# Performance work log

Hardware: AMD Instinct MI355X
Metric: run time of the kernel (lower is better)

Reference implementation:

```python
import jax, jax.numpy as jnp
import numpy as np

# Solver constants (from HopfieldLayer.__init__ / RKF56Solver(dt, tol=0.01, min_dt=0.1))
DT0 = 0.1
TOL = 0.01
MIN_DT = 0.1
MAX_STEPS = 32       # cap on adaptive iterations (fixed-length scan, masked)
SPEED_TOL = 1e-3     # stop_condition: |dx/dt|_inf below this => converged


def inverse_boundary_reflect(x):
    # y = x on even integer cells, 1 - x on odd cells; plain autodiff gives the
    # same VJP as the tf.custom_gradient (dy vs -dy) since the int cast is
    # only used in the predicate.
    i = x.astype(jnp.int32)
    return jnp.where(i % 2 == 0, x, 1.0 - x)


def make_pvf(W, b):
    def energy(y):
        # classic Hopfield energy, summed over batch: -0.5 y^T W y - b.y
        return -0.5 * jnp.einsum('bi,ij,bj->', y, W, y) - jnp.sum(y @ b)

    def pvf(x):  # phase vector field: -grad_x E(G^{-1}(x))
        return -jax.grad(lambda z: energy(inverse_boundary_reflect(z)))(x)

    return pvf


def _hopfield_forward(x0, W, b):
    f = make_pvf(W, b)

    def body(carry, _):
        x, dt, t, done = carry
        # Runge-Kutta-Fehlberg 6-stage embedded pair (4th/5th order)
        k1 = f(x)
        k2 = f(x + dt * (0.25 * k1))
        k3 = f(x + dt * (3.0 / 32.0 * k1 + 9.0 / 32.0 * k2))
        k4 = f(x + dt * (1932.0 / 2197.0 * k1 - 7200.0 / 2197.0 * k2 + 7296.0 / 2197.0 * k3))
        k5 = f(x + dt * (439.0 / 216.0 * k1 - 8.0 * k2 + 3680.0 / 513.0 * k3 - 845.0 / 4104.0 * k4))
        k6 = f(x + dt * (-8.0 / 27.0 * k1 + 2.0 * k2 - 3544.0 / 2565.0 * k3 + 1859.0 / 4104.0 * k4 - 11.0 / 40.0 * k5))
        x5 = x + dt * (16.0 / 135.0 * k1 + 6656.0 / 12825.0 * k3 + 28561.0 / 56430.0 * k4 - 9.0 / 50.0 * k5 + 2.0 / 55.0 * k6)
        x4 = x + dt * (25.0 / 216.0 * k1 + 1408.0 / 2565.0 * k3 + 2197.0 / 4104.0 * k4 - 1.0 / 5.0 * k5)
        err = jnp.max(jnp.abs(x5 - x4))
        accept = err < TOL
        step = jnp.logical_and(accept, jnp.logical_not(done))
        x_new = jnp.where(step, x5, x)
        t_new = jnp.where(step, t + dt, t)
        # stop condition: effective speed of accepted step below threshold
        speed = jnp.max(jnp.abs(x5 - x)) / dt
        done_new = jnp.logical_or(done, jnp.logical_and(step, speed < SPEED_TOL))
        # adaptive step-size control (non-differentiable, as in the TF solver)
        scale = 0.9 * (TOL / (jax.lax.stop_gradient(err) + 1e-12)) ** 0.2
        dt_new = jnp.maximum(dt * jnp.clip(scale, 0.1, 4.0), MIN_DT)
        dt_new = jnp.where(done, dt, dt_new)
        return (x_new, dt_new, t_new, done_new), None

    init = (x0,
            jnp.asarray(DT0, x0.dtype),
            jnp.asarray(0.0, x0.dtype),
            jnp.asarray(False))
    (x1, _, _, _), _ = jax.lax.scan(body, init, None, length=MAX_STEPS)
    return x1


def setup_inputs() -> dict:
    key = jax.random.key(0)
    kx, kw, kb = jax.random.split(key, 3)
    B, D = 512, 2048
    x0 = jax.random.uniform(kx, (B, D), dtype=jnp.float32)
    W = jax.random.normal(kw, (D, D), dtype=jnp.float32) / np.sqrt(D)
    W = 0.5 * (W + W.T)  # symmetric Hopfield coupling
    b = 0.1 * jax.random.normal(kb, (D,), dtype=jnp.float32)
    return {"x0": x0, "W": W, "b": b}


def reference(x0, W, b):
    return _hopfield_forward(x0, W, b)
```

## Files before the change

kernel.cpp:

```cpp
#include <hip/hip_runtime.h>

#define DDIM 2048
#define BDIM 512
#define NELEM (BDIM * DDIM)
#define NV4 (NELEM / 4)
#define NW4 (DDIM * DDIM / 4)

#define SC_DT 0
#define SC_DONE 1
#define SC_ERR 2
#define SC_SP 3
#define SC_COMMIT 4

#define TOLF 0.01f
#define MIN_DTF 0.1f
#define SPEED_TOLF 1e-3f

typedef _Float16 half8 __attribute__((ext_vector_type(8)));
typedef _Float16 half4v __attribute__((ext_vector_type(4)));
typedef float f32x4 __attribute__((ext_vector_type(4)));

__device__ __forceinline__ void glds16(const _Float16* g, _Float16* l) {
    __builtin_amdgcn_global_load_lds((__attribute__((address_space(1))) void*)g,
                                     (__attribute__((address_space(3))) void*)l, 16, 0, 0);
}

__device__ __forceinline__ void split_f16(float y, _Float16& h, _Float16& l) {
    h = (_Float16)y;
    l = (_Float16)(y - (float)h);
}

__device__ __forceinline__ float reflect_f(float v) {
    int i = (int)v;
    return ((i & 1) == 0) ? v : 1.0f - v;
}


__global__ void wconv_kernel(const float* __restrict__ W, _Float16* __restrict__ Wh,
                             _Float16* __restrict__ Wl) {
    int tid = blockIdx.x * blockDim.x + threadIdx.x;
    const float4* Wv = (const float4*)W;
    for (int i = tid; i < NW4; i += gridDim.x * blockDim.x) {
        float4 v = Wv[i];
        half4v h, l;
        float vv[4] = {v.x, v.y, v.z, v.w};
#pragma unroll
        for (int q = 0; q < 4; ++q) {
            _Float16 hh, ll;
            split_f16(vv[q], hh, ll);
            h[q] = hh;
            l[q] = ll;
        }
        *(half4v*)&Wh[(size_t)i * 4] = h;
        *(half4v*)&Wl[(size_t)i * 4] = l;
    }
}

__global__ void init_kernel(const float* __restrict__ x0, float* __restrict__ x,
                            _Float16* __restrict__ Ah, _Float16* __restrict__ Al,
                            float* __restrict__ scal) {
    int tid = blockIdx.x * blockDim.x + threadIdx.x;
    const float4* X0 = (const float4*)x0;
    float4* X = (float4*)x;
    for (int i = tid; i < NV4; i += gridDim.x * blockDim.x) {
        float4 v = X0[i];
        X[i] = v;
        half4v h, l;
        float vv[4] = {v.x, v.y, v.z, v.w};
#pragma unroll
        for (int q = 0; q < 4; ++q) {
            float y = reflect_f(vv[q]);
            _Float16 hh, ll;
            split_f16(y, hh, ll);
            h[q] = hh;
            l[q] = ll;
        }
        *(half4v*)&Ah[(size_t)i * 4] = h;
        *(half4v*)&Al[(size_t)i * 4] = l;
    }
    if (tid == 0) {
        scal[SC_DT] = 0.1f;
        ((unsigned int*)scal)[SC_DONE] = 0u;
        scal[SC_ERR] = 0.0f;
        scal[SC_SP] = 0.0f;
        ((unsigned int*)scal)[SC_COMMIT] = 0u;
    }
}


template <int S>
__global__ __launch_bounds__(512, 2) void stage_kernel(
    const _Float16* __restrict__ Ah, const _Float16* __restrict__ Al,
    _Float16* __restrict__ Aoh, _Float16* __restrict__ Aol, const _Float16* __restrict__ Wh,
    const _Float16* __restrict__ Wl, const float* __restrict__ bias,
    const float* __restrict__ xg, const float* __restrict__ gk1, const float* __restrict__ gk2,
    const float* __restrict__ gk3, const float* __restrict__ gk4, const float* __restrict__ gk5,
    float* __restrict__ kout, float* __restrict__ x5out, float* __restrict__ scal) {
    __shared__ __align__(16) _Float16 lds[2][2][4][64 * 64];
    __shared__ float serr[8], ssp[8];

    const int tid = threadIdx.x;
    const int li = tid & 63;
    const int wid = tid >> 6;
    const int g = wid >> 2;
    const int w4 = wid & 3;
    const int wm = w4 >> 1, wn = w4 & 1;

    const int bid = blockIdx.x;
    const int xcd = bid & 7, jj = bid >> 3;
    const int bm = (xcd & 1) * 4 + (jj & 3);
    const int bn = (xcd >> 1) * 8 + (jj >> 2);

    f32x4 acc[2][2];
#pragma unroll
    for (int a = 0; a < 2; ++a)
#pragma unroll
        for (int b = 0; b < 2; ++b) acc[a][b] = (f32x4)(0.0f);

    auto stage4 = [&](int buf, int k0) {
#pragma unroll
        for (int cc = 0; cc < 2; ++cc) {
            int c = w4 + cc * 4;
            int row = c * 8 + (li >> 3);
            int clog = (li & 7) ^ (row & 7);
            int ga = (bm * 64 + row) * DDIM + k0 + clog * 8;
            int gw = (bn * 64 + row) * DDIM + k0 + clog * 8;
            int lo = c * 512 + li * 8;
            glds16(Ah + ga, &lds[g][buf][0][lo]);
            glds16(Al + ga, &lds[g][buf][1][lo]);
            glds16(Wh + gw, &lds[g][buf][2][lo]);
            glds16(Wl + gw, &lds[g][buf][3][lo]);
        }
    };

    auto rdfrag = [&](int buf, int mat, int rbase, int ks) -> half8 {
        int r = rbase + (li & 15);
        int cl = ks * 4 + (li >> 4);
        int off = r * 64 + ((cl ^ (r & 7)) << 3);
        return *(const half8*)&lds[g][buf][mat][off];
    };

    auto compute = [&](int buf) {
#pragma unroll
        for (int ks = 0; ks < 2; ++ks) {
            half8 ah[2], al[2], bh[2], bl[2];
#pragma unroll
            for (int f = 0; f < 2; ++f) {
                ah[f] = rdfrag(buf, 0, wm * 32 + f * 16, ks);
                al[f] = rdfrag(buf, 1, wm * 32 + f * 16, ks);
                bh[f] = rdfrag(buf, 2, wn * 32 + f * 16, ks);
                bl[f] = rdfrag(buf, 3, wn * 32 + f * 16, ks);
            }
#pragma unroll
            for (int mi = 0; mi < 2; ++mi)
#pragma unroll
                for (int ni = 0; ni < 2; ++ni) {
                    acc[mi][ni] = __builtin_amdgcn_mfma_f32_16x16x32_f16(ah[mi], bh[ni],
                                                                         acc[mi][ni], 0, 0, 0);
                    acc[mi][ni] = __builtin_amdgcn_mfma_f32_16x16x32_f16(ah[mi], bl[ni],
                                                                         acc[mi][ni], 0, 0, 0);
                    acc[mi][ni] = __builtin_amdgcn_mfma_f32_16x16x32_f16(al[mi], bh[ni],
                                                                         acc[mi][ni], 0, 0, 0);
                }
        }
    };

    const int kbase = g * 1024;
    stage4(0, kbase);
#pragma unroll 2
    for (int t = 0; t < 16; ++t) {
        if (t + 1 < 16) {
            stage4((t + 1) & 1, kbase + (t + 1) * 64);
            asm volatile("s_waitcnt vmcnt(8)" ::: "memory");
        } else {
            asm volatile("s_waitcnt vmcnt(0)" ::: "memory");
        }
        __builtin_amdgcn_sched_barrier(0);
        __builtin_amdgcn_s_barrier();
        compute(t & 1);
        __builtin_amdgcn_s_barrier();
    }

    float4* xch = (float4*)&lds[0][0][0][0];
#pragma unroll
    for (int ni = 0; ni < 2; ++ni) {
        int slot = ((g * 4 + w4) * 2 + ni) * 64 + li;
        if (g == 0)
            xch[slot] = make_float4(acc[1][ni][0], acc[1][ni][1], acc[1][ni][2], acc[1][ni][3]);
        else
            xch[slot] = make_float4(acc[0][ni][0], acc[0][ni][1], acc[0][ni][2], acc[0][ni][3]);
    }
    __syncthreads();
    f32x4 fin[2];
#pragma unroll
    for (int ni = 0; ni < 2; ++ni) {
        int slot = (((1 - g) * 4 + w4) * 2 + ni) * 64 + li;
        float4 p = xch[slot];
        f32x4 mine = (g == 0) ? acc[0][ni] : acc[1][ni];
        mine[0] += p.x;
        mine[1] += p.y;
        mine[2] += p.z;
        mine[3] += p.w;
        fin[ni] = mine;
    }

    const float dt = scal[SC_DT];
    const int lrow = li >> 4, lcol = li & 15;
    const float bias0 = bias[bn * 64 + wn * 32 + lcol];
    const float bias1 = bias[bn * 64 + wn * 32 + 16 + lcol];
    float lerr = 0.0f, lsp = 0.0f;

#pragma unroll
    for (int r = 0; r < 4; ++r) {
        int m = bm * 64 + wm * 32 + g * 16 + lrow * 4 + r;
        size_t base = (size_t)m * DDIM;
#pragma unroll
        for (int ni = 0; ni < 2; ++ni) {
            int n = bn * 64 + wn * 32 + ni * 16 + lcol;
            size_t idx = base + n;
            float accv = fin[ni][r] + (ni == 0 ? bias0 : bias1);
            float xv = xg[idx];
            float lk1 = 0.f, lk2 = 0.f, lk3 = 0.f, lk4 = 0.f, lk5 = 0.f;
            if constexpr (S >= 2) lk1 = gk1[idx];
            if constexpr (S >= 3) lk2 = gk2[idx];
            if constexpr (S >= 4) lk3 = gk3[idx];
            if constexpr (S >= 5) lk4 = gk4[idx];
            if constexpr (S >= 6) lk5 = gk5[idx];
            float xs;
            if constexpr (S == 1) xs = xv;
            if constexpr (S == 2) xs = xv + dt * (0.25f * lk1);
            if constexpr (S == 3)
                xs = xv + dt * ((float)(3.0 / 32.0) * lk1 + (float)(9.0 / 32.0) * lk2);
            if constexpr (S == 4)
                xs = xv + dt * ((float)(1932.0 / 2197.0) * lk1 + (float)(-7200.0 / 2197.0) * lk2 +
                                (float)(7296.0 / 2197.0) * lk3);
            if constexpr (S == 5)
                xs = xv + dt * ((float)(439.0 / 216.0) * lk1 - 8.0f * lk2 +
                                (float)(3680.0 / 513.0) * lk3 + (float)(-845.0 / 4104.0) * lk4);
            if constexpr (S == 6)
                xs = xv + dt * ((float)(-8.0 / 27.0) * lk1 + 2.0f * lk2 +
                                (float)(-3544.0 / 2565.0) * lk3 + (float)(1859.0 / 4104.0) * lk4 +
                                (float)(-11.0 / 40.0) * lk5);
            float sgn = (((int)xs) & 1) ? -1.0f : 1.0f;
            float kv = sgn * accv;
            if constexpr (S < 6) {
                kout[idx] = kv;
                float xn;
                if constexpr (S == 1) xn = xv + dt * (0.25f * kv);
                if constexpr (S == 2)
                    xn = xv + dt * ((float)(3.0 / 32.0) * lk1 + (float)(9.0 / 32.0) * kv);
                if constexpr (S == 3)
                    xn = xv + dt * ((float)(1932.0 / 2197.0) * lk1 +
                                    (float)(-7200.0 / 2197.0) * lk2 + (float)(7296.0 / 2197.0) * kv);
                if constexpr (S == 4)
                    xn = xv + dt * ((float)(439.0 / 216.0) * lk1 - 8.0f * lk2 +
                                    (float)(3680.0 / 513.0) * lk3 + (float)(-845.0 / 4104.0) * kv);
                if constexpr (S == 5)
                    xn = xv + dt * ((float)(-8.0 / 27.0) * lk1 + 2.0f * lk2 +
                                    (float)(-3544.0 / 2565.0) * lk3 +
                                    (float)(1859.0 / 4104.0) * lk4 + (float)(-11.0 / 40.0) * kv);
                float y = reflect_f(xn);
                _Float16 hh, ll;
                split_f16(y, hh, ll);
                Aoh[idx] = hh;
                Aol[idx] = ll;
            } else {
                float x5 = xv + dt * ((float)(16.0 / 135.0) * lk1 + (float)(6656.0 / 12825.0) * lk3 +
                                      (float)(28561.0 / 56430.0) * lk4 + (float)(-9.0 / 50.0) * lk5 +
                                      (float)(2.0 / 55.0) * kv);
                float x4 = xv + dt * ((float)(25.0 / 216.0) * lk1 + (float)(1408.0 / 2565.0) * lk3 +
                                      (float)(2197.0 / 4104.0) * lk4 + (float)(-1.0 / 5.0) * lk5);
                lerr = fmaxf(lerr, fabsf(x5 - x4));
                lsp = fmaxf(lsp, fabsf(x5 - xv));
                x5out[idx] = x5;
            }
        }
    }

    if constexpr (S == 6) {
#pragma unroll
        for (int off = 32; off > 0; off >>= 1) {
            lerr = fmaxf(lerr, __shfl_down(lerr, off));
            lsp = fmaxf(lsp, __shfl_down(lsp, off));
        }
        if (li == 0) {
            serr[wid] = lerr;
            ssp[wid] = lsp;
        }
        __syncthreads();
        if (tid == 0) {
            float e = serr[0], s = ssp[0];
#pragma unroll
            for (int w = 1; w < 8; ++w) {
                e = fmaxf(e, serr[w]);
                s = fmaxf(s, ssp[w]);
            }
            atomicMax((unsigned int*)&scal[SC_ERR], __float_as_uint(e));
            atomicMax((unsigned int*)&scal[SC_SP], __float_as_uint(s));
        }
    }
}


__global__ void scalar_update(float* scal) {
    if (threadIdx.x == 0 && blockIdx.x == 0) {
        float dt = scal[SC_DT];
        float err = scal[SC_ERR];
        float spmax = scal[SC_SP];
        unsigned int done = ((unsigned int*)scal)[SC_DONE];
        bool accept = err < TOLF;
        bool step = accept && (done == 0u);
        float speed = spmax / dt;
        unsigned int done_new = (done || (step && (speed < SPEED_TOLF))) ? 1u : 0u;
        float scale = 0.9f * powf(TOLF / (err + 1e-12f), 0.2f);
        scale = fminf(fmaxf(scale, 0.1f), 4.0f);
        float dtn = fmaxf(dt * scale, MIN_DTF);
        scal[SC_DT] = done ? dt : dtn;
        ((unsigned int*)scal)[SC_DONE] = done_new;
        ((unsigned int*)scal)[SC_COMMIT] = step ? 1u : 0u;
        scal[SC_ERR] = 0.0f;
        scal[SC_SP] = 0.0f;
    }
}

__global__ void commit_prep(float* __restrict__ x, const float* __restrict__ x5,
                            _Float16* __restrict__ Ah, _Float16* __restrict__ Al,
                            const float* __restrict__ scal) {
    bool com = ((const unsigned int*)scal)[SC_COMMIT] != 0u;
    int tid = blockIdx.x * blockDim.x + threadIdx.x;
    float4* X = (float4*)x;
    const float4* X5 = (const float4*)x5;
    for (int i = tid; i < NV4; i += gridDim.x * blockDim.x) {
        float4 v = com ? X5[i] : X[i];
        if (com) X[i] = v;
        half4v h, l;
        float vv[4] = {v.x, v.y, v.z, v.w};
#pragma unroll
        for (int q = 0; q < 4; ++q) {
            float y = reflect_f(vv[q]);
            _Float16 hh, ll;
            split_f16(y, hh, ll);
            h[q] = hh;
            l[q] = ll;
        }
        *(half4v*)&Ah[(size_t)i * 4] = h;
        *(half4v*)&Al[(size_t)i * 4] = l;
    }
}


extern "C" void kernel_launch(void* const* d_in, const int* in_sizes, int n_in, void* d_out,
                              int out_size, void* d_ws, size_t ws_size, hipStream_t stream) {
    const float* x0 = (const float*)d_in[0];
    const float* W = (const float*)d_in[1];
    const float* bias = (const float*)d_in[2];
    float* x = (float*)d_out;

    float* ws = (float*)d_ws;
    float* k1 = ws + 0 * (size_t)NELEM;
    float* k2 = ws + 1 * (size_t)NELEM;
    float* k3 = ws + 2 * (size_t)NELEM;
    float* k4 = ws + 3 * (size_t)NELEM;
    float* k5 = ws + 4 * (size_t)NELEM;
    float* x5 = ws + 5 * (size_t)NELEM;
    float* scal = ws + 6 * (size_t)NELEM;
    _Float16* hb = (_Float16*)(ws + 6 * (size_t)NELEM + 64);
    _Float16* A0h = hb + 0 * (size_t)NELEM;
    _Float16* A0l = hb + 1 * (size_t)NELEM;
    _Float16* A1h = hb + 2 * (size_t)NELEM;
    _Float16* A1l = hb + 3 * (size_t)NELEM;
    _Float16* Wh = hb + 4 * (size_t)NELEM;
    _Float16* Wl = Wh + (size_t)DDIM * DDIM;

    wconv_kernel<<<2048, 256, 0, stream>>>(W, Wh, Wl);
    init_kernel<<<1024, 256, 0, stream>>>(x0, x, A1h, A1l, scal);

    for (int it = 0; it < 32; ++it) {
        stage_kernel<1><<<256, 512, 0, stream>>>(A1h, A1l, A0h, A0l, Wh, Wl, bias, x, k1, k2, k3,
                                                 k4, k5, k1, x5, scal);
        stage_kernel<2><<<256, 512, 0, stream>>>(A0h, A0l, A1h, A1l, Wh, Wl, bias, x, k1, k2, k3,
                                                 k4, k5, k2, x5, scal);
        stage_kernel<3><<<256, 512, 0, stream>>>(A1h, A1l, A0h, A0l, Wh, Wl, bias, x, k1, k2, k3,
                                                 k4, k5, k3, x5, scal);
        stage_kernel<4><<<256, 512, 0, stream>>>(A0h, A0l, A1h, A1l, Wh, Wl, bias, x, k1, k2, k3,
                                                 k4, k5, k4, x5, scal);
        stage_kernel<5><<<256, 512, 0, stream>>>(A1h, A1l, A0h, A0l, Wh, Wl, bias, x, k1, k2, k3,
                                                 k4, k5, k5, x5, scal);
        stage_kernel<6><<<256, 512, 0, stream>>>(A0h, A0l, A1h, A1l, Wh, Wl, bias, x, k1, k2, k3,
                                                 k4, k5, k1, x5, scal);
        scalar_update<<<1, 64, 0, stream>>>(scal);
        commit_prep<<<1024, 256, 0, stream>>>(x, x5, A1h, A1l, scal);
    }
}
```

Baseline: 4.139 ms.

## Load low-half fragments directly to registers, fuse scalar update into commit

The low-precision halves of A and W no longer go through LDS. Each wave loads them straight from global memory into registers as MFMA fragments, and only the high halves are staged via global_load_lds. This halves LDS footprint and LDS read traffic, and adds s_setprio around the MFMA blocks. The scalar_update kernel is folded into the commit kernel using ping-pong scalar slots, and commit is skipped entirely on rejected steps because the x-derived fp16 buffer is kept separate from the stage ping-pong buffers. The direct global loads are less coalesced and add register pressure.

```diff
diff --git a/kernel.cpp b/kernel.cpp
--- a/kernel.cpp
+++ b/kernel.cpp
@@ -10,7 +10,6 @@
 #define SC_DONE 1
 #define SC_ERR 2
 #define SC_SP 3
-#define SC_COMMIT 4
 
 #define TOLF 0.01f
 #define MIN_DTF 0.1f
@@ -57,7 +56,7 @@
 }
 
 __global__ void init_kernel(const float* __restrict__ x0, float* __restrict__ x,
-                            _Float16* __restrict__ Ah, _Float16* __restrict__ Al,
+                            _Float16* __restrict__ Axh, _Float16* __restrict__ Axl,
                             float* __restrict__ scal) {
     int tid = blockIdx.x * blockDim.x + threadIdx.x;
     const float4* X0 = (const float4*)x0;
@@ -75,15 +74,16 @@
             h[q] = hh;
             l[q] = ll;
         }
-        *(half4v*)&Ah[(size_t)i * 4] = h;
-        *(half4v*)&Al[(size_t)i * 4] = l;
+        *(half4v*)&Axh[(size_t)i * 4] = h;
+        *(half4v*)&Axl[(size_t)i * 4] = l;
     }
     if (tid == 0) {
         scal[SC_DT] = 0.1f;
         ((unsigned int*)scal)[SC_DONE] = 0u;
         scal[SC_ERR] = 0.0f;
         scal[SC_SP] = 0.0f;
-        ((unsigned int*)scal)[SC_COMMIT] = 0u;
+        scal[8 + SC_ERR] = 0.0f;
+        scal[8 + SC_SP] = 0.0f;
     }
 }
 
@@ -96,7 +96,7 @@
     const float* __restrict__ xg, const float* __restrict__ gk1, const float* __restrict__ gk2,
     const float* __restrict__ gk3, const float* __restrict__ gk4, const float* __restrict__ gk5,
     float* __restrict__ kout, float* __restrict__ x5out, float* __restrict__ scal) {
-    __shared__ __align__(16) _Float16 lds[2][2][4][64 * 64];
+    __shared__ __align__(16) _Float16 lds[2][2][2][64 * 64];
     __shared__ float serr[8], ssp[8];
 
     const int tid = threadIdx.x;
@@ -111,13 +111,20 @@
     const int bm = (xcd & 1) * 4 + (jj & 3);
     const int bn = (xcd >> 1) * 8 + (jj >> 2);
 
+    const int kbase = g * 1024;
+
     f32x4 acc[2][2];
 #pragma unroll
     for (int a = 0; a < 2; ++a)
 #pragma unroll
         for (int b = 0; b < 2; ++b) acc[a][b] = (f32x4)(0.0f);
 
-    auto stage4 = [&](int buf, int k0) {
+    const _Float16* Al_base =
+        Al + (size_t)(bm * 64 + wm * 32 + (li & 15)) * DDIM + kbase + ((li >> 4) << 3);
+    const _Float16* Wl_base =
+        Wl + (size_t)(bn * 64 + wn * 32 + (li & 15)) * DDIM + kbase + ((li >> 4) << 3);
+
+    auto stage_hi = [&](int buf, int k0) {
 #pragma unroll
         for (int cc = 0; cc < 2; ++cc) {
             int c = w4 + cc * 4;
@@ -125,11 +132,21 @@
             int clog = (li & 7) ^ (row & 7);
             int ga = (bm * 64 + row) * DDIM + k0 + clog * 8;
             int gw = (bn * 64 + row) * DDIM + k0 + clog * 8;
-            int lo = c * 512 + li * 8;
-            glds16(Ah + ga, &lds[g][buf][0][lo]);
-            glds16(Al + ga, &lds[g][buf][1][lo]);
-            glds16(Wh + gw, &lds[g][buf][2][lo]);
-            glds16(Wl + gw, &lds[g][buf][3][lo]);
+            int lo_ = c * 512 + li * 8;
+            glds16(Ah + ga, &lds[g][buf][0][lo_]);
+            glds16(Wh + gw, &lds[g][buf][1][lo_]);
+        }
+    };
+
+    auto load_lo = [&](half8(&lo)[8], int t) {
+#pragma unroll
+        for (int ks = 0; ks < 2; ++ks) {
+#pragma unroll
+            for (int mi = 0; mi < 2; ++mi)
+                lo[ks * 2 + mi] = *(const half8*)(Al_base + (size_t)mi * 16 * DDIM + t * 64 + ks * 32);
+#pragma unroll
+            for (int ni = 0; ni < 2; ++ni)
+                lo[4 + ks * 2 + ni] = *(const half8*)(Wl_base + (size_t)ni * 16 * DDIM + t * 64 + ks * 32);
         }
     };
 
@@ -140,44 +157,54 @@
         return *(const half8*)&lds[g][buf][mat][off];
     };
 
-    auto compute = [&](int buf) {
+    auto compute = [&](int buf, half8(&lo)[8]) {
 #pragma unroll
         for (int ks = 0; ks < 2; ++ks) {
-            half8 ah[2], al[2], bh[2], bl[2];
+            half8 ah[2], bh[2];
 #pragma unroll
             for (int f = 0; f < 2; ++f) {
                 ah[f] = rdfrag(buf, 0, wm * 32 + f * 16, ks);
-                al[f] = rdfrag(buf, 1, wm * 32 + f * 16, ks);
-                bh[f] = rdfrag(buf, 2, wn * 32 + f * 16, ks);
-                bl[f] = rdfrag(buf, 3, wn * 32 + f * 16, ks);
+                bh[f] = rdfrag(buf, 1, wn * 32 + f * 16, ks);
             }
+            __builtin_amdgcn_s_setprio(1);
 #pragma unroll
             for (int mi = 0; mi < 2; ++mi)
 #pragma unroll
                 for (int ni = 0; ni < 2; ++ni) {
                     acc[mi][ni] = __builtin_amdgcn_mfma_f32_16x16x32_f16(ah[mi], bh[ni],
                                                                          acc[mi][ni], 0, 0, 0);
-                    acc[mi][ni] = __builtin_amdgcn_mfma_f32_16x16x32_f16(ah[mi], bl[ni],
-                                                                         acc[mi][ni], 0, 0, 0);
-                    acc[mi][ni] = __builtin_amdgcn_mfma_f32_16x16x32_f16(al[mi], bh[ni],
-                                                                         acc[mi][ni], 0, 0, 0);
+                    acc[mi][ni] = __builtin_amdgcn_mfma_f32_16x16x32_f16(
+                        ah[mi], lo[4 + ks * 2 + ni], acc[mi][ni], 0, 0, 0);
+                    acc[mi][ni] = __builtin_amdgcn_mfma_f32_16x16x32_f16(
+                        lo[ks * 2 + mi], bh[ni], acc[mi][ni], 0, 0, 0);
                 }
+            __builtin_amdgcn_s_setprio(0);
         }
     };
 
-    const int kbase = g * 1024;
-    stage4(0, kbase);
-#pragma unroll 2
-    for (int t = 0; t < 16; ++t) {
-        if (t + 1 < 16) {
-            stage4((t + 1) & 1, kbase + (t + 1) * 64);
-            asm volatile("s_waitcnt vmcnt(8)" ::: "memory");
+    half8 loA[8], loB[8];
+    stage_hi(0, kbase);
+    load_lo(loA, 0);
+#pragma unroll 1
+    for (int tt = 0; tt < 8; ++tt) {
+        const int t0 = tt * 2;
+        stage_hi(1, kbase + (t0 + 1) * 64);
+        load_lo(loB, t0 + 1);
+        asm volatile("s_waitcnt vmcnt(12)" ::: "memory");
+        __builtin_amdgcn_sched_barrier(0);
+        __builtin_amdgcn_s_barrier();
+        compute(0, loA);
+        __builtin_amdgcn_s_barrier();
+        if (tt < 7) {
+            stage_hi(0, kbase + (t0 + 2) * 64);
+            load_lo(loA, t0 + 2);
+            asm volatile("s_waitcnt vmcnt(12)" ::: "memory");
         } else {
             asm volatile("s_waitcnt vmcnt(0)" ::: "memory");
         }
         __builtin_amdgcn_sched_barrier(0);
         __builtin_amdgcn_s_barrier();
-        compute(t & 1);
+        compute(1, loB);
         __builtin_amdgcn_s_barrier();
     }
 
@@ -302,37 +329,33 @@
 }
 
 
-__global__ void scalar_update(float* scal) {
-    if (threadIdx.x == 0 && blockIdx.x == 0) {
-        float dt = scal[SC_DT];
-        float err = scal[SC_ERR];
-        float spmax = scal[SC_SP];
-        unsigned int done = ((unsigned int*)scal)[SC_DONE];
-        bool accept = err < TOLF;
-        bool step = accept && (done == 0u);
-        float speed = spmax / dt;
-        unsigned int done_new = (done || (step && (speed < SPEED_TOLF))) ? 1u : 0u;
-        float scale = 0.9f * powf(TOLF / (err + 1e-12f), 0.2f);
-        scale = fminf(fmaxf(scale, 0.1f), 4.0f);
-        float dtn = fmaxf(dt * scale, MIN_DTF);
-        scal[SC_DT] = done ? dt : dtn;
-        ((unsigned int*)scal)[SC_DONE] = done_new;
-        ((unsigned int*)scal)[SC_COMMIT] = step ? 1u : 0u;
-        scal[SC_ERR] = 0.0f;
-        scal[SC_SP] = 0.0f;
-    }
-}
-
-__global__ void commit_prep(float* __restrict__ x, const float* __restrict__ x5,
-                            _Float16* __restrict__ Ah, _Float16* __restrict__ Al,
-                            const float* __restrict__ scal) {
-    bool com = ((const unsigned int*)scal)[SC_COMMIT] != 0u;
+__global__ void commit_fused(float* __restrict__ x, const float* __restrict__ x5,
+                             _Float16* __restrict__ Axh, _Float16* __restrict__ Axl,
+                             const float* __restrict__ scal_rd, float* __restrict__ scal_wr) {
+    float dt = scal_rd[SC_DT];
+    float err = scal_rd[SC_ERR];
+    float sp = scal_rd[SC_SP];
+    unsigned int done = ((const unsigned int*)scal_rd)[SC_DONE];
+    bool accept = err < TOLF;
+    bool step = accept && (done == 0u);
+    float speed = sp / dt;
+    unsigned int done_new = (done || (step && speed < SPEED_TOLF)) ? 1u : 0u;
+    float scale = 0.9f * powf(TOLF / (err + 1e-12f), 0.2f);
+    scale = fminf(fmaxf(scale, 0.1f), 4.0f);
+    float dtn = fmaxf(dt * scale, MIN_DTF);
+    if (blockIdx.x == 0 && threadIdx.x == 0) {
+        scal_wr[SC_DT] = done ? dt : dtn;
+        ((unsigned int*)scal_wr)[SC_DONE] = done_new;
+        scal_wr[SC_ERR] = 0.0f;
+        scal_wr[SC_SP] = 0.0f;
+    }
+    if (!step) return;
     int tid = blockIdx.x * blockDim.x + threadIdx.x;
     float4* X = (float4*)x;
     const float4* X5 = (const float4*)x5;
     for (int i = tid; i < NV4; i += gridDim.x * blockDim.x) {
-        float4 v = com ? X5[i] : X[i];
-        if (com) X[i] = v;
+        float4 v = X5[i];
+        X[i] = v;
         half4v h, l;
         float vv[4] = {v.x, v.y, v.z, v.w};
 #pragma unroll
@@ -343,8 +366,8 @@
             h[q] = hh;
             l[q] = ll;
         }
-        *(half4v*)&Ah[(size_t)i * 4] = h;
-        *(half4v*)&Al[(size_t)i * 4] = l;
+        *(half4v*)&Axh[(size_t)i * 4] = h;
+        *(half4v*)&Axl[(size_t)i * 4] = l;
     }
 }
 
@@ -365,30 +388,33 @@
     float* x5 = ws + 5 * (size_t)NELEM;
     float* scal = ws + 6 * (size_t)NELEM;
     _Float16* hb = (_Float16*)(ws + 6 * (size_t)NELEM + 64);
-    _Float16* A0h = hb + 0 * (size_t)NELEM;
-    _Float16* A0l = hb + 1 * (size_t)NELEM;
-    _Float16* A1h = hb + 2 * (size_t)NELEM;
-    _Float16* A1l = hb + 3 * (size_t)NELEM;
-    _Float16* Wh = hb + 4 * (size_t)NELEM;
+    _Float16* Axh = hb + 0 * (size_t)NELEM;
+    _Float16* Axl = hb + 1 * (size_t)NELEM;
+    _Float16* P0h = hb + 2 * (size_t)NELEM;
+    _Float16* P0l = hb + 3 * (size_t)NELEM;
+    _Float16* P1h = hb + 4 * (size_t)NELEM;
+    _Float16* P1l = hb + 5 * (size_t)NELEM;
+    _Float16* Wh = hb + 6 * (size_t)NELEM;
     _Float16* Wl = Wh + (size_t)DDIM * DDIM;
 
     wconv_kernel<<<2048, 256, 0, stream>>>(W, Wh, Wl);
-    init_kernel<<<1024, 256, 0, stream>>>(x0, x, A1h, A1l, scal);
+    init_kernel<<<1024, 256, 0, stream>>>(x0, x, Axh, Axl, scal);
 
     for (int it = 0; it < 32; ++it) {
-        stage_kernel<1><<<256, 512, 0, stream>>>(A1h, A1l, A0h, A0l, Wh, Wl, bias, x, k1, k2, k3,
-                                                 k4, k5, k1, x5, scal);
-        stage_kernel<2><<<256, 512, 0, stream>>>(A0h, A0l, A1h, A1l, Wh, Wl, bias, x, k1, k2, k3,
-                                                 k4, k5, k2, x5, scal);
-        stage_kernel<3><<<256, 512, 0, stream>>>(A1h, A1l, A0h, A0l, Wh, Wl, bias, x, k1, k2, k3,
-                                                 k4, k5, k3, x5, scal);
-        stage_kernel<4><<<256, 512, 0, stream>>>(A0h, A0l, A1h, A1l, Wh, Wl, bias, x, k1, k2, k3,
-                                                 k4, k5, k4, x5, scal);
-        stage_kernel<5><<<256, 512, 0, stream>>>(A1h, A1l, A0h, A0l, Wh, Wl, bias, x, k1, k2, k3,
-                                                 k4, k5, k5, x5, scal);
-        stage_kernel<6><<<256, 512, 0, stream>>>(A0h, A0l, A1h, A1l, Wh, Wl, bias, x, k1, k2, k3,
-                                                 k4, k5, k1, x5, scal);
-        scalar_update<<<1, 64, 0, stream>>>(scal);
-        commit_prep<<<1024, 256, 0, stream>>>(x, x5, A1h, A1l, scal);
-    }
-}
+        float* sp = scal + (it & 1) * 8;
+        float* sn = scal + ((it + 1) & 1) * 8;
+        stage_kernel<1><<<256, 512, 0, stream>>>(Axh, Axl, P0h, P0l, Wh, Wl, bias, x, k1, k2, k3,
+                                                 k4, k5, k1, x5, sp);
+        stage_kernel<2><<<256, 512, 0, stream>>>(P0h, P0l, P1h, P1l, Wh, Wl, bias, x, k1, k2, k3,
+                                                 k4, k5, k2, x5, sp);
+        stage_kernel<3><<<256, 512, 0, stream>>>(P1h, P1l, P0h, P0l, Wh, Wl, bias, x, k1, k2, k3,
+                                                 k4, k5, k3, x5, sp);
+        stage_kernel<4><<<256, 512, 0, stream>>>(P0h, P0l, P1h, P1l, Wh, Wl, bias, x, k1, k2, k3,
+                                                 k4, k5, k4, x5, sp);
+        stage_kernel<5><<<256, 512, 0, stream>>>(P1h, P1l, P0h, P0l, Wh, Wl, bias, x, k1, k2, k3,
+                                                 k4, k5, k5, x5, sp);
+        stage_kernel<6><<<256, 512, 0, stream>>>(P0h, P0l, P1h, P1l, Wh, Wl, bias, x, k1, k2, k3,
+                                                 k4, k5, k1, x5, sp);
+        commit_fused<<<1024, 256, 0, stream>>>(x, x5, Axh, Axl, sp, sn);
+    }
+}
```

Result: slower. 8.190 ms (+97.9%).
